# Kernel tuning notes

Hardware: AMD Instinct MI355X
Metric: run time of the kernel (lower is better)

## Reference

```python
import jax, jax.numpy as jnp
import numpy as np

N_USERS = 50000
N_ITEMS = 50000
N_NODES = N_USERS + N_ITEMS
N_EDGES = 1600000
D_IN = 128
D_OUT = 128


def setup_inputs() -> dict:
    key = jax.random.key(0)
    k1, k2, k3, k4, k5, k6 = jax.random.split(key, 6)
    u_f = jax.random.normal(k1, (N_USERS, D_IN), dtype=jnp.float32)
    v_f = jax.random.normal(k2, (N_ITEMS, D_IN), dtype=jnp.float32)
    adj_rows = jax.random.randint(k3, (N_EDGES,), 0, N_NODES, dtype=jnp.int32)
    adj_cols = jax.random.randint(k4, (N_EDGES,), 0, N_NODES, dtype=jnp.int32)
    adj_vals = jax.random.uniform(k5, (N_EDGES,), dtype=jnp.float32)
    # xavier_uniform init for weight [in_feats, out_feats]
    bound = float(np.sqrt(6.0 / (D_IN + D_OUT)))
    weight = jax.random.uniform(k6, (D_IN, D_OUT), dtype=jnp.float32,
                                minval=-bound, maxval=bound)
    return {"u_f": u_f, "v_f": v_f, "adj_rows": adj_rows,
            "adj_cols": adj_cols, "adj_vals": adj_vals, "weight": weight}


def reference(u_f, v_f, adj_rows, adj_cols, adj_vals, weight):
    # node_f = cat([u_f, v_f]) @ W          -- dense transform
    node_f = jnp.concatenate([u_f, v_f], axis=0)          # [N, D_in]
    node_f = node_f @ weight                               # [N, D_out]
    # sparse adjacency matmul: out[r] = sum_e vals[e] * node_f[cols[e]]
    msgs = adj_vals[:, None] * node_f[adj_cols]            # [E, D_out]
    out = jax.ops.segment_sum(msgs, adj_rows, num_segments=N_NODES)
    # activation (relu)
    return jax.nn.relu(out)
```

## Files before the change

kernel.cpp:

```cpp
#include <hip/hip_runtime.h>
#include <hip/hip_bf16.h>
#include <hip/hip_fp16.h>

#define N_USERS 50000
#define N_NODES 100000
#define N_EDGES 1600000
#define DIM 128
#define CAP 64

#define RPB 128
#define NBINS ((N_NODES + RPB - 1) / RPB)
#define BINCAP 4096
#define EPB 8192
#define FILL_BLOCKS ((N_EDGES + EPB - 1) / EPB)
#define GEMM_BLOCKS 828
#define FUSED_GRID 1024
#define WFRAG_ELEMS (32 * 64 * 8)

typedef __attribute__((ext_vector_type(8))) _Float16 half8;
typedef __attribute__((ext_vector_type(4))) float f32x4;

__global__ void prep_kernel(const float* __restrict__ W,
                            _Float16* __restrict__ wfrag_g,
                            int* __restrict__ gcount) {
    if (blockIdx.x == 64) {
        for (int b = threadIdx.x; b < 1024; b += 256) gcount[b] = 0;
        return;
    }
    const int f   = blockIdx.x * 256 + threadIdx.x;
    const int ts  = f >> 9;
    const int rem = f & 511;
    const int ln  = rem >> 3;
    const int j   = rem & 7;
    const int t   = ts >> 2;
    const int s   = ts & 3;
    const int krow = s * 32 + (ln >> 4) * 8 + j;
    const int col  = t * 16 + (ln & 15);
    wfrag_g[f] = (_Float16)W[krow * DIM + col];
}

__device__ __forceinline__ void gemm_main(
        const float* __restrict__ u_f, const float* __restrict__ v_f,
        _Float16* __restrict__ node_f, const _Float16* wfrag,
        int blockId, int nBlocks) {
    const int tid  = threadIdx.x;
    const int lane = tid & 63;
    const int wave = tid >> 6;
    const int m    = lane & 15;
    const int quad = lane >> 4;
    const int n_wtiles = N_NODES / 16;

    for (int wt = blockId * 4 + wave; wt < n_wtiles; wt += nBlocks * 4) {
        const int row = wt * 16 + m;
        const float* src = (row < N_USERS) ? u_f + (size_t)row * DIM
                                           : v_f + (size_t)(row - N_USERS) * DIM;
        f32x4 acc[8];
        #pragma unroll
        for (int t = 0; t < 8; ++t) acc[t] = (f32x4){0.f, 0.f, 0.f, 0.f};

        #pragma unroll
        for (int s = 0; s < 4; ++s) {
            const float* ap = src + s * 32 + quad * 8;
            const float4 a0 = *(const float4*)ap;
            const float4 a1 = *(const float4*)(ap + 4);
            half8 af;
            af[0] = (_Float16)a0.x; af[1] = (_Float16)a0.y;
            af[2] = (_Float16)a0.z; af[3] = (_Float16)a0.w;
            af[4] = (_Float16)a1.x; af[5] = (_Float16)a1.y;
            af[6] = (_Float16)a1.z; af[7] = (_Float16)a1.w;
            #pragma unroll
            for (int t = 0; t < 8; ++t) {
                const half8 wf = *(const half8*)&wfrag[((t * 4 + s) * 64 + lane) * 8];
                acc[t] = __builtin_amdgcn_mfma_f32_16x16x32_f16(af, wf, acc[t], 0, 0, 0);
            }
        }

        const int base = wt * 16;
        #pragma unroll
        for (int t = 0; t < 8; ++t) {
            #pragma unroll
            for (int r = 0; r < 4; ++r) {
                const int orow = base + quad * 4 + r;
                node_f[(size_t)orow * DIM + t * 16 + m] = (_Float16)acc[t][r];
            }
        }
    }
}

__global__ __launch_bounds__(256) void fused_gemm_fill_kernel(
        const float* __restrict__ u_f, const float* __restrict__ v_f,
        const _Float16* __restrict__ wfrag_g, _Float16* __restrict__ node_f,
        const int* __restrict__ rows, const int* __restrict__ cols,
        const float* __restrict__ vals,
        int* __restrict__ gcount, long long* __restrict__ bin_data) {
    __shared__ union {
        _Float16 wfrag[WFRAG_ELEMS];
        struct { int hist[NBINS]; int base_[NBINS]; } a;
    } sh;

    if (blockIdx.x >= FILL_BLOCKS) {
        const int4* src = (const int4*)wfrag_g;
        int4* dst = (int4*)sh.wfrag;
        #pragma unroll
        for (int i = 0; i < WFRAG_ELEMS / 8 / 256; ++i)
            dst[i * 256 + threadIdx.x] = src[i * 256 + threadIdx.x];
        __syncthreads();
        gemm_main(u_f, v_f, node_f, sh.wfrag,
                  blockIdx.x - FILL_BLOCKS, GEMM_BLOCKS);
        return;
    }

    const int bb  = blockIdx.x;
    const int tid = threadIdx.x;
    const int e0  = bb * EPB;

    for (int b = tid; b < NBINS; b += 256) sh.a.hist[b] = 0;
    __syncthreads();

    unsigned meta[EPB / 256];
    #pragma unroll
    for (int i = 0; i < EPB / 256; ++i) {
        const int e = e0 + i * 256 + tid;
        if (e < N_EDGES) {
            const int row = rows[e];
            const int bin = row >> 7;
            const int pos = atomicAdd(&sh.a.hist[bin], 1);
            meta[i] = ((unsigned)bin << 20) | ((unsigned)(row & 127) << 13)
                    | (unsigned)pos;
        } else {
            meta[i] = 0xFFFFFFFFu;
        }
    }
    __syncthreads();

    for (int b = tid; b < NBINS; b += 256) {
        const int h = sh.a.hist[b];
        sh.a.base_[b] = h ? atomicAdd(&gcount[b], h) : 0;
    }
    __syncthreads();

    #pragma unroll
    for (int i = 0; i < EPB / 256; ++i) {
        if (meta[i] == 0xFFFFFFFFu) continue;
        const int e   = e0 + i * 256 + tid;
        const int bin = meta[i] >> 20;
        const int rl  = (meta[i] >> 13) & 127;
        const int pos = meta[i] & 0x1FFF;
        const int idx = sh.a.base_[bin] + pos;
        if (idx < BINCAP) {
            const unsigned w0 = ((unsigned)rl << 17) | (unsigned)cols[e];
            const long long ent =
                ((long long)__float_as_int(vals[e]) << 32) | (long long)w0;
            bin_data[(size_t)bin * BINCAP + idx] = ent;
        }
    }
}

__global__ __launch_bounds__(256) void gemm_mfma_kernel(
        const float* __restrict__ u_f, const float* __restrict__ v_f,
        const float* __restrict__ W, _Float16* __restrict__ node_f) {
    __shared__ _Float16 wfrag[WFRAG_ELEMS];
    const int tid = threadIdx.x;
    for (int f = tid * 64, end = tid * 64 + 64; f < end; ++f) {
        const int ts   = f >> 9;
        const int rem  = f & 511;
        const int ln   = rem >> 3;
        const int j    = rem & 7;
        const int t    = ts >> 2;
        const int s    = ts & 3;
        const int krow = s * 32 + (ln >> 4) * 8 + j;
        const int col  = t * 16 + (ln & 15);
        wfrag[f] = (_Float16)W[krow * DIM + col];
    }
    __syncthreads();
    gemm_main(u_f, v_f, node_f, wfrag, blockIdx.x, gridDim.x);
}

__device__ __forceinline__ void gather_issue(
        const _Float16* __restrict__ node_f,
        const unsigned (*list)[CAP], const int* rowcnt,
        int nrows, int wave, int lane, int pid, int cl, int rp,
        int& cnt, int& col, float& val, half8 h[4]) {
    const int rl = rp * 16 + wave;
    if (rp >= 8 || rl >= nrows) { cnt = -1; return; }
    int c_ = rowcnt[rl]; if (c_ > CAP) c_ = CAP;
    cnt = c_;
    const unsigned p = (lane < c_) ? list[rl][lane] : 0u;
    col = (int)(p & 0x1FFFFu);
    val = (float)(p >> 17) * (1.f / 32767.f);
    #pragma unroll
    for (int q = 0; q < 4; ++q) {
        const int j  = q * 4 + pid;
        const int sj = j < c_ ? j : 0;
        const int c  = __shfl(col, sj, 64);
        if (j < c_)
            h[q] = *(const half8*)&node_f[(size_t)c * DIM + cl * 8];
    }
}

__device__ __forceinline__ void gather_consume(
        const _Float16* __restrict__ node_f, float* __restrict__ out,
        int row0, int wave, int pid, int cl, int rp,
        int cnt, int col, float val, const half8 h[4]) {
    if (cnt < 0) return;
    const int row = row0 + rp * 16 + wave;

    float acc[8];
    #pragma unroll
    for (int i = 0; i < 8; ++i) acc[i] = 0.f;

    #pragma unroll
    for (int q = 0; q < 4; ++q) {
        const int j  = q * 4 + pid;
        const int sj = j < cnt ? j : 0;
        const float v = __shfl(val, sj, 64);
        if (j < cnt) {
            #pragma unroll
            for (int i = 0; i < 8; ++i) acc[i] += v * (float)h[q][i];
        }
    }
    for (int j = 16; j < cnt; j += 4) {
        const int jj = j + pid;
        const int sj = jj < cnt ? jj : 0;
        const int   c = __shfl(col, sj, 64);
        const float v = __shfl(val, sj, 64);
        if (jj < cnt) {
            const half8 hh = *(const half8*)&node_f[(size_t)c * DIM + cl * 8];
            #pragma unroll
            for (int i = 0; i < 8; ++i) acc[i] += v * (float)hh[i];
        }
    }

    #pragma unroll
    for (int i = 0; i < 8; ++i) {
        acc[i] += __shfl_xor(acc[i], 16, 64);
        acc[i] += __shfl_xor(acc[i], 32, 64);
    }

    if (pid == 0) {
        f32x4 r0, r1;
        #pragma unroll
        for (int i = 0; i < 4; ++i) {
            r0[i] = acc[i]     > 0.f ? acc[i]     : 0.f;
            r1[i] = acc[i + 4] > 0.f ? acc[i + 4] : 0.f;
        }
        float* dst = &out[(size_t)row * DIM + cl * 8];
        __builtin_nontemporal_store(r0, (f32x4*)dst);
        __builtin_nontemporal_store(r1, (f32x4*)(dst + 4));
    }
}

__global__ __launch_bounds__(1024, 8) void bin_gather_kernel(
        const _Float16* __restrict__ node_f, const int* __restrict__ gcount,
        const long long* __restrict__ bin_data, float* __restrict__ out) {
    __shared__ unsigned list[RPB][CAP];
    __shared__ int rowcnt[RPB];

    const int bin  = blockIdx.x;
    const int tid  = threadIdx.x;
    const int row0 = bin * RPB;
    const int nrows = (N_NODES - row0 < RPB) ? (N_NODES - row0) : RPB;

    if (tid < RPB) rowcnt[tid] = 0;
    __syncthreads();

    int n = gcount[bin];
    if (n > BINCAP) n = BINCAP;
    for (int k = tid; k < n; k += 1024) {
        const long long ent = bin_data[(size_t)bin * BINCAP + k];
        const unsigned w0 = (unsigned)ent;
        const float v = __int_as_float((int)(ent >> 32));
        const int rl = (int)(w0 >> 17);
        const int pos = atomicAdd(&rowcnt[rl], 1);
        if (pos < CAP) {
            const int q = (int)(v * 32767.f + 0.5f);
            list[rl][pos] = ((unsigned)q << 17) | (w0 & 0x1FFFFu);
        }
    }
    __syncthreads();

    const int wave = tid >> 6;
    const int lane = tid & 63;
    const int pid  = lane >> 4;
    const int cl   = lane & 15;

    int cntA, colA; float valA; half8 hA[4];
    int cntB, colB; float valB; half8 hB[4];

    gather_issue(node_f, list, rowcnt, nrows, wave, lane, pid, cl, 0,
                 cntA, colA, valA, hA);
    #pragma unroll
    for (int rp = 0; rp < 8; rp += 2) {
        gather_issue(node_f, list, rowcnt, nrows, wave, lane, pid, cl, rp + 1,
                     cntB, colB, valB, hB);
        gather_consume(node_f, out, row0, wave, pid, cl, rp,
                       cntA, colA, valA, hA);
        gather_issue(node_f, list, rowcnt, nrows, wave, lane, pid, cl, rp + 2,
                     cntA, colA, valA, hA);
        gather_consume(node_f, out, row0, wave, pid, cl, rp + 1,
                       cntB, colB, valB, hB);
    }
}

__global__ void zero_out_kernel(float* __restrict__ out) {
    int i = blockIdx.x * blockDim.x + threadIdx.x;
    int idx = i * 4;
    if (idx < N_NODES * DIM) {
        float4 z = {0.f, 0.f, 0.f, 0.f};
        *(float4*)&out[idx] = z;
    }
}

__global__ void scatter_kernel(const _Float16* __restrict__ node_f,
                               const int* __restrict__ rows, const int* __restrict__ cols,
                               const float* __restrict__ vals, float* __restrict__ out) {
    int t = blockIdx.x * blockDim.x + threadIdx.x;
    int e = t >> 5;
    int part = t & 31;
    if (e >= N_EDGES) return;
    int r = rows[e], c = cols[e];
    float v = vals[e];
    const __half2 h0 = *(const __half2*)&node_f[(size_t)c * DIM + part * 4];
    const __half2 h1 = *(const __half2*)&node_f[(size_t)c * DIM + part * 4 + 2];
    const float2 f0 = __half22float2(h0);
    const float2 f1 = __half22float2(h1);
    float* dst = &out[(size_t)r * DIM + part * 4];
    unsafeAtomicAdd(dst + 0, v * f0.x);
    unsafeAtomicAdd(dst + 1, v * f0.y);
    unsafeAtomicAdd(dst + 2, v * f1.x);
    unsafeAtomicAdd(dst + 3, v * f1.y);
}

__global__ void relu_kernel(float* __restrict__ out) {
    int i = blockIdx.x * blockDim.x + threadIdx.x;
    int idx = i * 4;
    if (idx < N_NODES * DIM) {
        float4 v = *(float4*)&out[idx];
        v.x = v.x > 0.f ? v.x : 0.f;
        v.y = v.y > 0.f ? v.y : 0.f;
        v.z = v.z > 0.f ? v.z : 0.f;
        v.w = v.w > 0.f ? v.w : 0.f;
        *(float4*)&out[idx] = v;
    }
}

extern "C" void kernel_launch(void* const* d_in, const int* in_sizes, int n_in,
                              void* d_out, int out_size, void* d_ws, size_t ws_size,
                              hipStream_t stream) {
    const float* u_f  = (const float*)d_in[0];
    const float* v_f  = (const float*)d_in[1];
    const int*   rows = (const int*)d_in[2];
    const int*   cols = (const int*)d_in[3];
    const float* vals = (const float*)d_in[4];
    const float* W    = (const float*)d_in[5];
    float* out = (float*)d_out;

    char* ws = (char*)d_ws;
    const size_t nodef_bytes   = (size_t)N_NODES * DIM * 2;
    const size_t gcount_bytes  = 4096;
    const size_t bindata_bytes = (size_t)NBINS * BINCAP * 8;
    const size_t wfrag_bytes   = (size_t)WFRAG_ELEMS * 2;

    _Float16* node_f = (_Float16*)ws;
    int* gcount = (int*)(ws + nodef_bytes);
    long long* bin_data = (long long*)(ws + nodef_bytes + gcount_bytes);
    _Float16* wfrag_g = (_Float16*)(ws + nodef_bytes + gcount_bytes + bindata_bytes);

    if (ws_size >= nodef_bytes + gcount_bytes + bindata_bytes + wfrag_bytes) {
        prep_kernel<<<65, 256, 0, stream>>>(W, wfrag_g, gcount);
        fused_gemm_fill_kernel<<<FUSED_GRID, 256, 0, stream>>>(
            u_f, v_f, wfrag_g, node_f, rows, cols, vals, gcount, bin_data);
        bin_gather_kernel<<<NBINS, 1024, 0, stream>>>(
            node_f, gcount, bin_data, out);
    } else {
        gemm_mfma_kernel<<<512, 256, 0, stream>>>(u_f, v_f, W, node_f);
        zero_out_kernel<<<(N_NODES * DIM / 4 + 255) / 256, 256, 0, stream>>>(out);
        scatter_kernel<<<((size_t)N_EDGES * 32 + 255) / 256, 256, 0, stream>>>(
            node_f, rows, cols, vals, out);
        relu_kernel<<<(N_NODES * DIM / 4 + 255) / 256, 256, 0, stream>>>(out);
    }
}
```

Measured before the change: 281.4 us.

## Split GEMM into half-tile tasks with work stealing by fill blocks

```diff
diff --git a/kernel.cpp b/kernel.cpp
--- a/kernel.cpp
+++ b/kernel.cpp
@@ -13,9 +13,12 @@
 #define BINCAP 4096
 #define EPB 8192
 #define FILL_BLOCKS ((N_EDGES + EPB - 1) / EPB)
-#define GEMM_BLOCKS 828
-#define FUSED_GRID 1024
+#define GEMM_BLOCKS 1084
+#define FUSED_GRID 1280
 #define WFRAG_ELEMS (32 * 64 * 8)
+#define N_TASKS 12500
+#define TA_STATIC 10000
+#define STEAL_CTR 1000
 
 typedef __attribute__((ext_vector_type(8))) _Float16 half8;
 typedef __attribute__((ext_vector_type(4))) float f32x4;
@@ -39,51 +42,60 @@
     wfrag_g[f] = (_Float16)W[krow * DIM + col];
 }
 
-__device__ __forceinline__ void gemm_main(
+__device__ __forceinline__ void gemm_task(
         const float* __restrict__ u_f, const float* __restrict__ v_f,
         _Float16* __restrict__ node_f, const _Float16* wfrag,
-        int blockId, int nBlocks) {
-    const int tid  = threadIdx.x;
-    const int lane = tid & 63;
-    const int wave = tid >> 6;
+        int task, int lane) {
+    const int wt = task >> 1;
+    const int h  = task & 1;
     const int m    = lane & 15;
     const int quad = lane >> 4;
-    const int n_wtiles = N_NODES / 16;
-
-    for (int wt = blockId * 4 + wave; wt < n_wtiles; wt += nBlocks * 4) {
-        const int row = wt * 16 + m;
-        const float* src = (row < N_USERS) ? u_f + (size_t)row * DIM
-                                           : v_f + (size_t)(row - N_USERS) * DIM;
-        f32x4 acc[8];
+    const int row  = wt * 16 + m;
+    const float* src = (row < N_USERS) ? u_f + (size_t)row * DIM
+                                       : v_f + (size_t)(row - N_USERS) * DIM;
+    f32x4 acc[4];
+    #pragma unroll
+    for (int t = 0; t < 4; ++t) acc[t] = (f32x4){0.f, 0.f, 0.f, 0.f};
+
+    #pragma unroll
+    for (int s = 0; s < 4; ++s) {
+        const float* ap = src + s * 32 + quad * 8;
+        const float4 a0 = *(const float4*)ap;
+        const float4 a1 = *(const float4*)(ap + 4);
+        half8 af;
+        af[0] = (_Float16)a0.x; af[1] = (_Float16)a0.y;
+        af[2] = (_Float16)a0.z; af[3] = (_Float16)a0.w;
+        af[4] = (_Float16)a1.x; af[5] = (_Float16)a1.y;
+        af[6] = (_Float16)a1.z; af[7] = (_Float16)a1.w;
         #pragma unroll
-        for (int t = 0; t < 8; ++t) acc[t] = (f32x4){0.f, 0.f, 0.f, 0.f};
-
+        for (int tt = 0; tt < 4; ++tt) {
+            const int t = h * 4 + tt;
+            const half8 wf = *(const half8*)&wfrag[((t * 4 + s) * 64 + lane) * 8];
+            acc[tt] = __builtin_amdgcn_mfma_f32_16x16x32_f16(af, wf, acc[tt], 0, 0, 0);
+        }
+    }
+
+    const int base = wt * 16;
+    #pragma unroll
+    for (int tt = 0; tt < 4; ++tt) {
         #pragma unroll
-        for (int s = 0; s < 4; ++s) {
-            const float* ap = src + s * 32 + quad * 8;
-            const float4 a0 = *(const float4*)ap;
-            const float4 a1 = *(const float4*)(ap + 4);
-            half8 af;
-            af[0] = (_Float16)a0.x; af[1] = (_Float16)a0.y;
-            af[2] = (_Float16)a0.z; af[3] = (_Float16)a0.w;
-            af[4] = (_Float16)a1.x; af[5] = (_Float16)a1.y;
-            af[6] = (_Float16)a1.z; af[7] = (_Float16)a1.w;
-            #pragma unroll
-            for (int t = 0; t < 8; ++t) {
-                const half8 wf = *(const half8*)&wfrag[((t * 4 + s) * 64 + lane) * 8];
-                acc[t] = __builtin_amdgcn_mfma_f32_16x16x32_f16(af, wf, acc[t], 0, 0, 0);
-            }
-        }
-
-        const int base = wt * 16;
-        #pragma unroll
-        for (int t = 0; t < 8; ++t) {
-            #pragma unroll
-            for (int r = 0; r < 4; ++r) {
-                const int orow = base + quad * 4 + r;
-                node_f[(size_t)orow * DIM + t * 16 + m] = (_Float16)acc[t][r];
-            }
-        }
+        for (int r = 0; r < 4; ++r) {
+            const int orow = base + quad * 4 + r;
+            node_f[(size_t)orow * DIM + (h * 4 + tt) * 16 + m] = (_Float16)acc[tt][r];
+        }
+    }
+}
+
+__device__ __forceinline__ void gemm_steal(
+        const float* __restrict__ u_f, const float* __restrict__ v_f,
+        _Float16* __restrict__ node_f, const _Float16* wfrag,
+        int* __restrict__ steal_ctr, int lane) {
+    for (;;) {
+        int t = 0;
+        if (lane == 0) t = atomicAdd(steal_ctr, 1);
+        t = __shfl(t, 0, 64) + TA_STATIC;
+        if (t >= N_TASKS) break;
+        gemm_task(u_f, v_f, node_f, wfrag, t, lane);
     }
 }
 
@@ -98,20 +110,25 @@
         struct { int hist[NBINS]; int base_[NBINS]; } a;
     } sh;
 
+    const int tid  = threadIdx.x;
+    const int lane = tid & 63;
+    const int wave = tid >> 6;
+
     if (blockIdx.x >= FILL_BLOCKS) {
         const int4* src = (const int4*)wfrag_g;
         int4* dst = (int4*)sh.wfrag;
         #pragma unroll
         for (int i = 0; i < WFRAG_ELEMS / 8 / 256; ++i)
-            dst[i * 256 + threadIdx.x] = src[i * 256 + threadIdx.x];
+            dst[i * 256 + tid] = src[i * 256 + tid];
         __syncthreads();
-        gemm_main(u_f, v_f, node_f, sh.wfrag,
-                  blockIdx.x - FILL_BLOCKS, GEMM_BLOCKS);
+        const int bid = blockIdx.x - FILL_BLOCKS;
+        for (int task = bid * 4 + wave; task < TA_STATIC; task += GEMM_BLOCKS * 4)
+            gemm_task(u_f, v_f, node_f, sh.wfrag, task, lane);
+        gemm_steal(u_f, v_f, node_f, sh.wfrag, &gcount[STEAL_CTR], lane);
         return;
     }
 
     const int bb  = blockIdx.x;
-    const int tid = threadIdx.x;
     const int e0  = bb * EPB;
 
     for (int b = tid; b < NBINS; b += 256) sh.a.hist[b] = 0;
@@ -154,6 +171,17 @@
             bin_data[(size_t)bin * BINCAP + idx] = ent;
         }
     }
+
+    __syncthreads();
+    {
+        const int4* src = (const int4*)wfrag_g;
+        int4* dst = (int4*)sh.wfrag;
+        #pragma unroll
+        for (int i = 0; i < WFRAG_ELEMS / 8 / 256; ++i)
+            dst[i * 256 + tid] = src[i * 256 + tid];
+    }
+    __syncthreads();
+    gemm_steal(u_f, v_f, node_f, sh.wfrag, &gcount[STEAL_CTR], lane);
 }
 
 __global__ __launch_bounds__(256) void gemm_mfma_kernel(
@@ -173,7 +201,10 @@
         wfrag[f] = (_Float16)W[krow * DIM + col];
     }
     __syncthreads();
-    gemm_main(u_f, v_f, node_f, wfrag, blockIdx.x, gridDim.x);
+    const int lane = tid & 63;
+    const int wave = tid >> 6;
+    for (int task = blockIdx.x * 4 + wave; task < N_TASKS; task += gridDim.x * 4)
+        gemm_task(u_f, v_f, node_f, wfrag, task, lane);
 }
 
 __device__ __forceinline__ void gather_issue(
@@ -250,7 +281,7 @@
     }
 }
 
-__global__ __launch_bounds__(1024, 8) void bin_gather_kernel(
+__global__ __launch_bounds__(1024) void bin_gather_kernel(
         const _Float16* __restrict__ node_f, const int* __restrict__ gcount,
         const long long* __restrict__ bin_data, float* __restrict__ out) {
     __shared__ unsigned list[RPB][CAP];
```

Result: slower. 296.8 us (+5.5%).
